# Kernel optimization log

Measured on AMD Instinct MI355X. Metric: run time of the kernel, lower is better.

The kernel has to match this reference:

```python
import jax, jax.numpy as jnp
import numpy as np

B, T, D = 2, 4096, 1024
HQ, HKV, HD = 16, 4, 64   # 16 query heads, 4 KV heads (kv_groups=4), head_dim=64
WIN = 256                 # sliding window radius (left == right == 256)


def setup_inputs() -> dict:
    key = jax.random.key(0)
    ks = jax.random.split(key, 9)
    s = 0.02  # small init scale for stable softmax logits
    return {
        "x": jax.random.normal(ks[0], (B, T, D), jnp.float32),
        "wq": jax.random.normal(ks[1], (D, HQ * HD), jnp.float32) * s,
        "bq": jnp.zeros((HQ * HD,), jnp.float32),
        "wk": jax.random.normal(ks[2], (D, HKV * HD), jnp.float32) * s,
        "bk": jnp.zeros((HKV * HD,), jnp.float32),
        "wv": jax.random.normal(ks[3], (D, HKV * HD), jnp.float32) * s,
        "bv": jnp.zeros((HKV * HD,), jnp.float32),
        "wo": jax.random.normal(ks[4], (HQ * HD, D), jnp.float32) * s,
        "bo": jnp.zeros((D,), jnp.float32),
    }


def _banded_gqa(q, k, v, left, right):
    """Sliding-window GQA attention: query i attends keys in [i-left, i+right].
    Never materializes the full [B,H,T,T] score matrix; uses banded blocks."""
    Bq, Tq, Hq, d = q.shape
    Hkv = k.shape[2]
    G = Hq // Hkv                      # query heads per KV head
    bs = max(left, right)              # block size == window radius; T % bs == 0
    nb = Tq // bs
    # queries: [B, nb, bs, Hkv, G, d]
    qb = q.reshape(Bq, nb, bs, Hkv, G, d)
    # gather 3 neighboring key/value blocks per query block (pad one block each side)
    pad = ((0, 0), (bs, bs), (0, 0), (0, 0))
    idx = jnp.arange(nb)[:, None] * bs + jnp.arange(3 * bs)[None, :]  # into padded seq
    kctx = jnp.pad(k, pad)[:, idx]     # [B, nb, 3bs, Hkv, d]
    vctx = jnp.pad(v, pad)[:, idx]     # [B, nb, 3bs, Hkv, d]
    scale = 1.0 / jnp.sqrt(jnp.asarray(d, q.dtype))
    # banded scores: [B, nb, Hkv, G, bs, 3bs]
    scores = jnp.einsum('bnqhgd,bnkhd->bnhgqk', qb, kctx) * scale
    qpos = jnp.arange(nb)[:, None, None] * bs + jnp.arange(bs)[None, :, None]
    kpos = (jnp.arange(nb)[:, None, None] - 1) * bs + jnp.arange(3 * bs)[None, None, :]
    valid = (kpos >= 0) & (kpos < Tq) & (kpos >= qpos - left) & (kpos <= qpos + right)
    scores = jnp.where(valid[None, :, None, None, :, :], scores, jnp.asarray(-1e30, scores.dtype))
    p = jax.nn.softmax(scores, axis=-1)
    out = jnp.einsum('bnhgqk,bnkhd->bnqhgd', p, vctx)
    return out.reshape(Bq, Tq, Hq, d)


def reference(x, wq, bq, wk, bk, wv, bv, wo, bo):
    q = (x @ wq + bq).reshape(B, T, HQ, HD)
    k = (x @ wk + bk).reshape(B, T, HKV, HD)
    v = (x @ wv + bv).reshape(B, T, HKV, HD)
    y = _banded_gqa(q, k, v, WIN, WIN)       # [B, T, HQ, HD]
    y = y.reshape(B, T, HQ * HD)
    return y @ wo + bo                        # dropout=0.0, deterministic -> identity
```

## Files before the change

kernel.cpp:

```cpp
#include <hip/hip_runtime.h>

typedef unsigned short u16;
typedef u16 u16x4 __attribute__((ext_vector_type(4)));
typedef u16 u16x8 __attribute__((ext_vector_type(8)));
typedef __bf16 bf16x8 __attribute__((ext_vector_type(8)));
typedef float f32x4 __attribute__((ext_vector_type(4)));

#define DEVINL static __device__ __forceinline__

DEVINL u16 f2bf(float f) {
    unsigned u = __builtin_bit_cast(unsigned, f);
    u += 0x7fff + ((u >> 16) & 1);
    return (u16)(u >> 16);
}

DEVINL u16 pbf(float f) {
    unsigned u = __builtin_bit_cast(unsigned, f);
    return (u16)((u + 0x8000) >> 16);
}

DEVINL f32x4 mfma_bf16(u16x8 a, u16x8 b, f32x4 c) {
    return __builtin_amdgcn_mfma_f32_16x16x32_bf16(
        __builtin_bit_cast(bf16x8, a), __builtin_bit_cast(bf16x8, b), c, 0, 0, 0);
}

DEVINL void gload16(const void* g, void* lds) {
    __builtin_amdgcn_global_load_lds(
        (const __attribute__((address_space(1))) void*)g,
        (__attribute__((address_space(3))) void*)lds, 16, 0, 0);
}


DEVINL void twt_body(const float* __restrict__ src, u16* __restrict__ dst,
                     int N, int rowOff, int bx, int by, int tid, float (*t)[65]) {
    int k0 = bx * 64, n0 = by * 64;
#pragma unroll
    for (int j = 0; j < 16; j++) {
        int idx = j * 256 + tid; int r = idx >> 6, c = idx & 63;
        t[r][c] = src[(size_t)(k0 + r) * N + n0 + c];
    }
    __syncthreads();
#pragma unroll
    for (int j = 0; j < 16; j++) {
        int idx = j * 256 + tid; int r = idx >> 6, c = idx & 63;
        dst[(size_t)(rowOff + n0 + r) * 1024 + k0 + c] = f2bf(t[c][r]);
    }
}

__global__ void prep_kernel(const float* __restrict__ x,
                            const float* __restrict__ wq, const float* __restrict__ bq,
                            const float* __restrict__ wk, const float* __restrict__ bk,
                            const float* __restrict__ wv, const float* __restrict__ bv,
                            const float* __restrict__ wo,
                            u16* __restrict__ xb, u16* __restrict__ wqkvt,
                            u16* __restrict__ wot, float* __restrict__ bqkv) {
    __shared__ float t[64][65];
    int bid = blockIdx.x, tid = threadIdx.x;
    if (bid < 8192) {
        int idx = bid * 256 + tid;
        float4 a = ((const float4*)x)[idx];
        u16x4 o;
        o[0] = f2bf(a.x); o[1] = f2bf(a.y); o[2] = f2bf(a.z); o[3] = f2bf(a.w);
        ((u16x4*)xb)[idx] = o;
    } else if (bid < 8448) {
        int id = bid - 8192; twt_body(wq, wqkvt, 1024, 0, id & 15, id >> 4, tid, t);
    } else if (bid < 8512) {
        int id = bid - 8448; twt_body(wk, wqkvt, 256, 1024, id & 15, id >> 4, tid, t);
    } else if (bid < 8576) {
        int id = bid - 8512; twt_body(wv, wqkvt, 256, 1280, id & 15, id >> 4, tid, t);
    } else if (bid < 8832) {
        int id = bid - 8576; twt_body(wo, wot, 1024, 0, id & 15, id >> 4, tid, t);
    } else {
        int i = (bid - 8832) * 256 + tid;
        if (i < 1024) bqkv[i] = bq[i];
        else if (i < 1280) bqkv[i] = bk[i - 1024];
        else if (i < 1536) bqkv[i] = bv[i - 1280];
    }
}


template <bool F32OUT, bool VSPLIT>
__global__ __launch_bounds__(256, 2) void gemm_bt(
    const u16* __restrict__ A, const u16* __restrict__ Bt, void* __restrict__ Cp,
    const float* __restrict__ bias, u16* __restrict__ vt,
    int M, int N, int K, int qn, float qscale) {
    __shared__ __align__(16) u16 As[128 * 64];
    __shared__ __align__(16) u16 Bs[128 * 64];
    int tid = threadIdx.x; int l = tid & 63; int w = tid >> 6;

    int nwg = gridDim.x * gridDim.y;
    int lin = blockIdx.y * gridDim.x + blockIdx.x;
    int q_ = nwg >> 3, r_ = nwg & 7;
    int xcd = lin & 7, i_ = lin >> 3;
    int wgid = (xcd < r_ ? xcd * (q_ + 1) : r_ * (q_ + 1) + (xcd - r_) * q_) + i_;
    int m0 = (wgid / gridDim.x) * 128, n0 = (wgid % gridDim.x) * 128;

    int wm = (w >> 1) * 64, wn = (w & 1) * 64;
    f32x4 acc[4][4] = {};

    int srow[4], scol[4];
#pragma unroll
    for (int c = 0; c < 4; c++) {
        int b = (w * 4 + c) * 1024 + l * 16;
        int row = b >> 7, inner = b & 127;
        srow[c] = row;
        scol[c] = (inner ^ ((row & 7) << 4)) >> 1;
    }
    int nk = K >> 6;
    for (int kt = 0; kt < nk; ++kt) {
        int kb = kt << 6;
#pragma unroll
        for (int c = 0; c < 4; c++) {
            gload16(A + (size_t)(m0 + srow[c]) * K + kb + scol[c], (char*)As + (w * 4 + c) * 1024);
            gload16(Bt + (size_t)(n0 + srow[c]) * K + kb + scol[c], (char*)Bs + (w * 4 + c) * 1024);
        }
        __syncthreads();
#pragma unroll
        for (int kc = 0; kc < 2; ++kc) {
            int co = (kc * 32 + (l >> 4) * 8) * 2;
            u16x8 af[4], bf[4];
#pragma unroll
            for (int mf = 0; mf < 4; ++mf) {
                int row = wm + mf * 16 + (l & 15);
                af[mf] = *(const u16x8*)((const char*)As + row * 128 + (co ^ ((row & 7) << 4)));
            }
#pragma unroll
            for (int nf = 0; nf < 4; ++nf) {
                int row = wn + nf * 16 + (l & 15);
                bf[nf] = *(const u16x8*)((const char*)Bs + row * 128 + (co ^ ((row & 7) << 4)));
            }
#pragma unroll
            for (int mf = 0; mf < 4; ++mf)
#pragma unroll
                for (int nf = 0; nf < 4; ++nf)
                    acc[mf][nf] = mfma_bf16(af[mf], bf[nf], acc[mf][nf]);
        }
        __syncthreads();
    }
#pragma unroll
    for (int mf = 0; mf < 4; ++mf) {
#pragma unroll
        for (int nf = 0; nf < 4; ++nf) {
            int col = n0 + wn + nf * 16 + (l & 15);
            float bv = bias ? bias[col] : 0.0f;
            float scl = (col < qn) ? qscale : 1.0f;
            if (VSPLIT && col >= 1280) {
                int row0 = m0 + wm + mf * 16 + (l >> 4) * 4;
                int b_ = row0 >> 12, t_ = row0 & 4095;
                u16x4 pk;
#pragma unroll
                for (int r = 0; r < 4; r++) pk[r] = f2bf(acc[mf][nf][r] + bv);
                *(u16x4*)(vt + ((size_t)(b_ * 256 + (col - 1280)) << 12) + t_) = pk;
            } else {
#pragma unroll
                for (int r = 0; r < 4; r++) {
                    int row = m0 + wm + mf * 16 + (l >> 4) * 4 + r;
                    float v = (acc[mf][nf][r] + bv) * scl;
                    if (F32OUT) ((float*)Cp)[(size_t)row * N + col] = v;
                    else        ((u16*)Cp)[(size_t)row * N + col] = f2bf(v);
                }
            }
        }
    }
}


__global__ __launch_bounds__(512, 4) void attn_kernel(
    const u16* __restrict__ qkv, const u16* __restrict__ vt, u16* __restrict__ y) {
    __shared__ __align__(16) u16 Ks[64 * 64];
    __shared__ __align__(16) u16 Vs[64 * 64];
    __shared__ __align__(16) u16 Ps[8][16 * 64];
    int tid = threadIdx.x, l = tid & 63, w = tid >> 6;
    int qb = ((blockIdx.x & 7) << 3) | (blockIdx.x >> 3);
    int h = blockIdx.y >> 1, hp = blockIdx.y & 1, b = blockIdx.z;
    int qstart = qb * 64;
    size_t rowbase = (size_t)b * 4096;
    int hq = h * 4 + hp * 2 + (w >> 2);
    int qrow0 = (w & 3) * 16;

    u16x8 qf_[2];
#pragma unroll
    for (int kc = 0; kc < 2; ++kc)
        qf_[kc] = *(const u16x8*)(qkv + (rowbase + qstart + qrow0 + (l & 15)) * 1536
                                  + hq * 64 + kc * 32 + (l >> 4) * 8);

    f32x4 o[4] = {};
    float mrow = -__builtin_inff(), srow_ = 0.f;

    const u16* kbase_ptr = qkv + 1024 + h * 64;
    const u16* vbase_ptr = vt + (size_t)((b * 4 + h) * 64) * 4096;

    int sb_ = w * 1024 + l * 16;
    int g_row = sb_ >> 7, g_inner = sb_ & 127;
    int g_col = (g_inner ^ ((g_row & 7) << 4)) >> 1;

#pragma unroll
    for (int kstart = qstart - 256; kstart <= qstart + 256; kstart += 64) {
        if (kstart < 0 || kstart >= 4096) continue;
        gload16(kbase_ptr + (rowbase + kstart + g_row) * 1536 + g_col, (char*)Ks + w * 1024);
        gload16(vbase_ptr + (size_t)g_row * 4096 + kstart + g_col, (char*)Vs + w * 1024);
        __syncthreads();

        f32x4 st[4] = {};
#pragma unroll
        for (int kc = 0; kc < 2; ++kc) {
            int co = (kc * 32 + (l >> 4) * 8) * 2;
#pragma unroll
            for (int kf = 0; kf < 4; ++kf) {
                int row = kf * 16 + (l & 15);
                u16x8 kfr = *(const u16x8*)((const char*)Ks + row * 128 + (co ^ ((row & 7) << 4)));
                st[kf] = mfma_bf16(kfr, qf_[kc], st[kf]);
            }
        }

        bool mlo = (kstart == qstart - 256);
        bool mhi = (kstart == qstart + 256);

        int qoff = qrow0 + (l & 15);
        float pmax = -1e30f;
        float sv[4][4];
#pragma unroll
        for (int kf = 0; kf < 4; ++kf)
#pragma unroll
            for (int r = 0; r < 4; r++) {
                int koff = kf * 16 + (l >> 4) * 4 + r;
                float v = st[kf][r];
                if (mlo && koff < qoff) v = -1e30f;
                if (mhi && koff > qoff) v = -1e30f;
                sv[kf][r] = v;
                pmax = fmaxf(pmax, v);
            }
        pmax = fmaxf(pmax, __shfl_xor(pmax, 16));
        pmax = fmaxf(pmax, __shfl_xor(pmax, 32));

        bool resc = !__all(pmax - mrow <= 8.0f);
        float newm = resc ? fmaxf(mrow, pmax) : mrow;
        float psum = 0.f;
#pragma unroll
        for (int kf = 0; kf < 4; ++kf) {
            u16x4 pk;
#pragma unroll
            for (int r = 0; r < 4; r++) {
                float e = __builtin_amdgcn_exp2f(sv[kf][r] - newm);
                psum += e;
                pk[r] = pbf(e);
            }
            int row = l & 15;
            int keyc = kf * 16 + (l >> 4) * 4;
            *(u16x4*)((char*)Ps[w] + ((row * 128 + keyc * 2) ^ ((row & 7) << 4))) = pk;
        }
        psum += __shfl_xor(psum, 16);
        psum += __shfl_xor(psum, 32);
        if (resc) {
            float fs = __builtin_amdgcn_exp2f(mrow - newm);
            srow_ = srow_ * fs + psum;
            mrow = newm;
#pragma unroll
            for (int r = 0; r < 4; r++) {
                float fb = __shfl(fs, (l >> 4) * 4 + r);
#pragma unroll
                for (int nf = 0; nf < 4; ++nf) o[nf][r] *= fb;
            }
        } else {
            srow_ += psum;
        }

#pragma unroll
        for (int kc = 0; kc < 2; ++kc) {
            int co = (kc * 32 + (l >> 4) * 8) * 2;
            int prow = l & 15;
            u16x8 pa = *(const u16x8*)((const char*)Ps[w] + ((prow * 128 + co) ^ ((prow & 7) << 4)));
#pragma unroll
            for (int nf = 0; nf < 4; ++nf) {
                int row = nf * 16 + (l & 15);
                u16x8 vb = *(const u16x8*)((const char*)Vs + row * 128 + (co ^ ((row & 7) << 4)));
                o[nf] = mfma_bf16(pa, vb, o[nf]);
            }
        }
        __syncthreads();
    }

    float inv = 1.0f / srow_;
#pragma unroll
    for (int r = 0; r < 4; r++) {
        float sb = __shfl(inv, (l >> 4) * 4 + r);
        int row = qstart + qrow0 + (l >> 4) * 4 + r;
#pragma unroll
        for (int nf = 0; nf < 4; ++nf) {
            int col = hq * 64 + nf * 16 + (l & 15);
            y[(rowbase + row) * 1024 + col] = f2bf(o[nf][r] * sb);
        }
    }
}


extern "C" void kernel_launch(void* const* d_in, const int* in_sizes, int n_in,
                              void* d_out, int out_size, void* d_ws, size_t ws_size,
                              hipStream_t stream) {
    const float* x  = (const float*)d_in[0];
    const float* wq = (const float*)d_in[1];
    const float* bq = (const float*)d_in[2];
    const float* wk = (const float*)d_in[3];
    const float* bk = (const float*)d_in[4];
    const float* wv = (const float*)d_in[5];
    const float* bv = (const float*)d_in[6];
    const float* wo = (const float*)d_in[7];
    const float* bo = (const float*)d_in[8];
    float* out = (float*)d_out;

    char* p = (char*)d_ws;
    u16* xb     = (u16*)p;   p += (size_t)8192 * 1024 * 2;
    u16* wqkvt  = (u16*)p;   p += (size_t)1536 * 1024 * 2;
    u16* wot    = (u16*)p;   p += (size_t)1024 * 1024 * 2;
    float* bqkv = (float*)p; p += 8192;
    u16* qkvb   = (u16*)p;   p += (size_t)8192 * 1536 * 2;
    u16* vtb    = (u16*)p;   p += (size_t)512 * 4096 * 2;
    u16* yb     = (u16*)p;

    prep_kernel<<<8838, 256, 0, stream>>>(x, wq, bq, wk, bk, wv, bv, wo,
                                          xb, wqkvt, wot, bqkv);

    gemm_bt<false, true><<<dim3(12, 64), 256, 0, stream>>>(xb, wqkvt, qkvb, bqkv, vtb,
                                                           8192, 1536, 1024, 1024, 0.18033688f);
    attn_kernel<<<dim3(64, 8, 2), 512, 0, stream>>>(qkvb, vtb, yb);
    gemm_bt<true, false><<<dim3(8, 64), 256, 0, stream>>>(yb, wot, out, bo, nullptr,
                                                          8192, 1024, 1024, 0, 1.0f);
}
```

Measured before the change: 107.7 us.

## Restructure attention blocks to cover all GQA heads and double-buffer K/V tiles

Each attention block now processes 128 query rows for all four query heads sharing one KV head, so K/V tiles are loaded once per group instead of once per head pair. K/V tiles are double-buffered in shared memory with a prefetch of the next tile during compute, and per-subtile band checks skip tiles outside the window and avoid masking for interior tiles. The grid shrinks to 256 blocks with much higher register use per wave, which risks lower occupancy and poor load balance.

New measurement: 116.3 us. 1.08x slower.

```diff
diff --git a/kernel.cpp b/kernel.cpp
--- a/kernel.cpp
+++ b/kernel.cpp
@@ -165,27 +165,31 @@
 }
 
 
-__global__ __launch_bounds__(512, 4) void attn_kernel(
+__global__ __launch_bounds__(512) void attn_kernel(
     const u16* __restrict__ qkv, const u16* __restrict__ vt, u16* __restrict__ y) {
-    __shared__ __align__(16) u16 Ks[64 * 64];
-    __shared__ __align__(16) u16 Vs[64 * 64];
+    __shared__ __align__(16) u16 Ks[2][64 * 64];
+    __shared__ __align__(16) u16 Vs[2][64 * 64];
     __shared__ __align__(16) u16 Ps[8][16 * 64];
     int tid = threadIdx.x, l = tid & 63, w = tid >> 6;
-    int qb = ((blockIdx.x & 7) << 3) | (blockIdx.x >> 3);
-    int h = blockIdx.y >> 1, hp = blockIdx.y & 1, b = blockIdx.z;
-    int qstart = qb * 64;
+    int chunk = blockIdx.x, h = blockIdx.y, b = blockIdx.z;
+    int c0 = chunk * 128;
     size_t rowbase = (size_t)b * 4096;
-    int hq = h * 4 + hp * 2 + (w >> 2);
-    int qrow0 = (w & 3) * 16;
-
-    u16x8 qf_[2];
-#pragma unroll
-    for (int kc = 0; kc < 2; ++kc)
-        qf_[kc] = *(const u16x8*)(qkv + (rowbase + qstart + qrow0 + (l & 15)) * 1536
-                                  + hq * 64 + kc * 32 + (l >> 4) * 8);
-
-    f32x4 o[4] = {};
-    float mrow = -__builtin_inff(), srow_ = 0.f;
+    int head = w >> 1;
+    int hq = h * 4 + head;
+    int sub = w & 1;
+
+    u16x8 qf_[4][2];
+#pragma unroll
+    for (int j = 0; j < 4; ++j)
+#pragma unroll
+        for (int kc = 0; kc < 2; ++kc)
+            qf_[j][kc] = *(const u16x8*)(qkv + (rowbase + c0 + sub * 16 + j * 32 + (l & 15)) * 1536
+                                          + hq * 64 + kc * 32 + (l >> 4) * 8);
+
+    f32x4 o[4][4] = {};
+    float m_[4], s_[4];
+#pragma unroll
+    for (int j = 0; j < 4; ++j) { m_[j] = -__builtin_inff(); s_[j] = 0.f; }
 
     const u16* kbase_ptr = qkv + 1024 + h * 64;
     const u16* vbase_ptr = vt + (size_t)((b * 4 + h) * 64) * 4096;
@@ -194,101 +198,134 @@
     int g_row = sb_ >> 7, g_inner = sb_ & 127;
     int g_col = (g_inner ^ ((g_row & 7) << 4)) >> 1;
 
-#pragma unroll
-    for (int kstart = qstart - 256; kstart <= qstart + 256; kstart += 64) {
-        if (kstart < 0 || kstart >= 4096) continue;
-        gload16(kbase_ptr + (rowbase + kstart + g_row) * 1536 + g_col, (char*)Ks + w * 1024);
-        gload16(vbase_ptr + (size_t)g_row * 4096 + kstart + g_col, (char*)Vs + w * 1024);
+    int klo = c0 - 256; if (klo < 0) klo = 0;
+    int khi = c0 + 127 + 256; if (khi > 4095) khi = 4095;
+    khi &= ~63;
+    int nt = ((khi - klo) >> 6) + 1;
+
+#define STAGE(bufi, ks_)                                                                  \
+    do {                                                                                  \
+        gload16(kbase_ptr + (rowbase + (ks_) + g_row) * 1536 + g_col,                     \
+                (char*)Ks[bufi] + w * 1024);                                              \
+        gload16(vbase_ptr + (size_t)g_row * 4096 + (ks_) + g_col,                         \
+                (char*)Vs[bufi] + w * 1024);                                              \
+    } while (0)
+
+    STAGE(0, klo);
+    for (int t = 0; t < nt; ++t) {
+        int kstart = klo + (t << 6);
+        int par = t & 1;
         __syncthreads();
-
-        f32x4 st[4] = {};
-#pragma unroll
-        for (int kc = 0; kc < 2; ++kc) {
-            int co = (kc * 32 + (l >> 4) * 8) * 2;
+        if (t + 1 < nt) STAGE(par ^ 1, kstart + 64);
+        const char* Kb = (const char*)Ks[par];
+        const char* Vb = (const char*)Vs[par];
+
+#pragma unroll
+        for (int j = 0; j < 4; ++j) {
+            int qlo = c0 + sub * 16 + j * 32;
+            int qhi = qlo + 15;
+            if (kstart + 63 < qlo - 256 || kstart > qhi + 256) continue;
+
+            f32x4 st[4] = {};
+#pragma unroll
+            for (int kc = 0; kc < 2; ++kc) {
+                int co = (kc * 32 + (l >> 4) * 8) * 2;
+#pragma unroll
+                for (int kf = 0; kf < 4; ++kf) {
+                    int row = kf * 16 + (l & 15);
+                    u16x8 kfr = *(const u16x8*)(Kb + row * 128 + (co ^ ((row & 7) << 4)));
+                    st[kf] = mfma_bf16(kfr, qf_[j][kc], st[kf]);
+                }
+            }
+
+            bool interior = (kstart >= qhi - 256) && (kstart + 63 <= qlo + 256);
+            float pmax = -1e30f;
+            float sv[4][4];
+            if (interior) {
+#pragma unroll
+                for (int kf = 0; kf < 4; ++kf)
+#pragma unroll
+                    for (int r = 0; r < 4; r++) {
+                        sv[kf][r] = st[kf][r];
+                        pmax = fmaxf(pmax, sv[kf][r]);
+                    }
+            } else {
+                int qp = qlo + (l & 15);
+#pragma unroll
+                for (int kf = 0; kf < 4; ++kf)
+#pragma unroll
+                    for (int r = 0; r < 4; r++) {
+                        int koff = kstart + kf * 16 + (l >> 4) * 4 + r;
+                        float v = st[kf][r];
+                        if (koff < qp - 256 || koff > qp + 256) v = -1e30f;
+                        sv[kf][r] = v;
+                        pmax = fmaxf(pmax, v);
+                    }
+            }
+            pmax = fmaxf(pmax, __shfl_xor(pmax, 16));
+            pmax = fmaxf(pmax, __shfl_xor(pmax, 32));
+            pmax = fmaxf(pmax, -60.0f);
+
+            bool resc = !__all(pmax - m_[j] <= 8.0f);
+            float newm = resc ? fmaxf(m_[j], pmax) : m_[j];
+            float psum = 0.f;
 #pragma unroll
             for (int kf = 0; kf < 4; ++kf) {
-                int row = kf * 16 + (l & 15);
-                u16x8 kfr = *(const u16x8*)((const char*)Ks + row * 128 + (co ^ ((row & 7) << 4)));
-                st[kf] = mfma_bf16(kfr, qf_[kc], st[kf]);
-            }
-        }
-
-        bool mlo = (kstart == qstart - 256);
-        bool mhi = (kstart == qstart + 256);
-
-        int qoff = qrow0 + (l & 15);
-        float pmax = -1e30f;
-        float sv[4][4];
-#pragma unroll
-        for (int kf = 0; kf < 4; ++kf)
-#pragma unroll
-            for (int r = 0; r < 4; r++) {
-                int koff = kf * 16 + (l >> 4) * 4 + r;
-                float v = st[kf][r];
-                if (mlo && koff < qoff) v = -1e30f;
-                if (mhi && koff > qoff) v = -1e30f;
-                sv[kf][r] = v;
-                pmax = fmaxf(pmax, v);
-            }
-        pmax = fmaxf(pmax, __shfl_xor(pmax, 16));
-        pmax = fmaxf(pmax, __shfl_xor(pmax, 32));
-
-        bool resc = !__all(pmax - mrow <= 8.0f);
-        float newm = resc ? fmaxf(mrow, pmax) : mrow;
-        float psum = 0.f;
-#pragma unroll
-        for (int kf = 0; kf < 4; ++kf) {
-            u16x4 pk;
-#pragma unroll
-            for (int r = 0; r < 4; r++) {
-                float e = __builtin_amdgcn_exp2f(sv[kf][r] - newm);
-                psum += e;
-                pk[r] = pbf(e);
-            }
-            int row = l & 15;
-            int keyc = kf * 16 + (l >> 4) * 4;
-            *(u16x4*)((char*)Ps[w] + ((row * 128 + keyc * 2) ^ ((row & 7) << 4))) = pk;
-        }
-        psum += __shfl_xor(psum, 16);
-        psum += __shfl_xor(psum, 32);
-        if (resc) {
-            float fs = __builtin_amdgcn_exp2f(mrow - newm);
-            srow_ = srow_ * fs + psum;
-            mrow = newm;
-#pragma unroll
-            for (int r = 0; r < 4; r++) {
-                float fb = __shfl(fs, (l >> 4) * 4 + r);
-#pragma unroll
-                for (int nf = 0; nf < 4; ++nf) o[nf][r] *= fb;
-            }
-        } else {
-            srow_ += psum;
-        }
-
-#pragma unroll
-        for (int kc = 0; kc < 2; ++kc) {
-            int co = (kc * 32 + (l >> 4) * 8) * 2;
-            int prow = l & 15;
-            u16x8 pa = *(const u16x8*)((const char*)Ps[w] + ((prow * 128 + co) ^ ((prow & 7) << 4)));
+                u16x4 pk;
+#pragma unroll
+                for (int r = 0; r < 4; r++) {
+                    float e = __builtin_amdgcn_exp2f(sv[kf][r] - newm);
+                    psum += e;
+                    pk[r] = pbf(e);
+                }
+                int row = l & 15;
+                int keyc = kf * 16 + (l >> 4) * 4;
+                *(u16x4*)((char*)Ps[w] + ((row * 128 + keyc * 2) ^ ((row & 7) << 4))) = pk;
+            }
+            psum += __shfl_xor(psum, 16);
+            psum += __shfl_xor(psum, 32);
+            if (resc) {
+                float fs = __builtin_amdgcn_exp2f(m_[j] - newm);
+                s_[j] = s_[j] * fs + psum;
+                m_[j] = newm;
+#pragma unroll
+                for (int r = 0; r < 4; r++) {
+                    float fb = __shfl(fs, (l >> 4) * 4 + r);
+#pragma unroll
+                    for (int nf = 0; nf < 4; ++nf) o[j][nf][r] *= fb;
+                }
+            } else {
+                s_[j] += psum;
+            }
+
+#pragma unroll
+            for (int kc = 0; kc < 2; ++kc) {
+                int co = (kc * 32 + (l >> 4) * 8) * 2;
+                int prow = l & 15;
+                u16x8 pa = *(const u16x8*)((const char*)Ps[w] + ((prow * 128 + co) ^ ((prow & 7) << 4)));
+#pragma unroll
+                for (int nf = 0; nf < 4; ++nf) {
+                    int row = nf * 16 + (l & 15);
+                    u16x8 vb = *(const u16x8*)(Vb + row * 128 + (co ^ ((row & 7) << 4)));
+                    o[j][nf] = mfma_bf16(pa, vb, o[j][nf]);
+                }
+            }
+        }
+    }
+#undef STAGE
+
+#pragma unroll
+    for (int j = 0; j < 4; ++j) {
+        float inv = 1.0f / s_[j];
+#pragma unroll
+        for (int r = 0; r < 4; r++) {
+            float sb = __shfl(inv, (l >> 4) * 4 + r);
+            int row = c0 + sub * 16 + j * 32 + (l >> 4) * 4 + r;
 #pragma unroll
             for (int nf = 0; nf < 4; ++nf) {
-                int row = nf * 16 + (l & 15);
-                u16x8 vb = *(const u16x8*)((const char*)Vs + row * 128 + (co ^ ((row & 7) << 4)));
-                o[nf] = mfma_bf16(pa, vb, o[nf]);
-            }
-        }
-        __syncthreads();
-    }
-
-    float inv = 1.0f / srow_;
-#pragma unroll
-    for (int r = 0; r < 4; r++) {
-        float sb = __shfl(inv, (l >> 4) * 4 + r);
-        int row = qstart + qrow0 + (l >> 4) * 4 + r;
-#pragma unroll
-        for (int nf = 0; nf < 4; ++nf) {
-            int col = hq * 64 + nf * 16 + (l & 15);
-            y[(rowbase + row) * 1024 + col] = f2bf(o[nf][r] * sb);
+                int col = hq * 64 + nf * 16 + (l & 15);
+                y[(rowbase + row) * 1024 + col] = f2bf(o[j][nf][r] * sb);
+            }
         }
     }
 }
@@ -322,7 +359,7 @@
 
     gemm_bt<false, true><<<dim3(12, 64), 256, 0, stream>>>(xb, wqkvt, qkvb, bqkv, vtb,
                                                            8192, 1536, 1024, 1024, 0.18033688f);
-    attn_kernel<<<dim3(64, 8, 2), 512, 0, stream>>>(qkvb, vtb, yb);
+    attn_kernel<<<dim3(32, 4, 2), 512, 0, stream>>>(qkvb, vtb, yb);
     gemm_bt<true, false><<<dim3(8, 64), 256, 0, stream>>>(yb, wot, out, bo, nullptr,
                                                           8192, 1024, 1024, 0, 1.0f);
 }
```
